# Performance work log

Hardware: AMD Instinct MI355X
Metric: run time of the kernel (lower is better)

The kernel has to match this reference:

```python
import jax, jax.numpy as jnp
import numpy as np

K = 20          # num neighbors (init kwarg k)
BN_EPS = 1e-5   # PyTorch BatchNorm default eps


def setup_inputs() -> dict:
    key = jax.random.key(0)
    k1, k2 = jax.random.split(key, 2)
    x = jax.random.normal(k1, (8, 64, 4096), dtype=jnp.float32)       # (b, d, n)
    w = jax.random.normal(k2, (64, 128), dtype=jnp.float32) * 0.05    # Conv2d 1x1: (out=64, in=2*64)
    gamma = jnp.ones((64,), jnp.float32)    # BatchNorm1d weight
    beta = jnp.zeros((64,), jnp.float32)    # BatchNorm1d bias
    return {"x": x, "w": w, "gamma": gamma, "beta": beta}


def reference(x, w, gamma, beta):
    # x: (b, d, n)
    xt = jnp.swapaxes(x, 1, 2)                       # (b, n, d)
    # kNN via pairwise squared euclidean distance (same ordering as torch.cdist)
    sq = jnp.sum(xt * xt, axis=-1)                   # (b, n)
    d2 = sq[:, :, None] + sq[:, None, :] - 2.0 * jnp.einsum('bnd,bmd->bnm', xt, xt)
    _, idx = jax.lax.top_k(-d2, K)                   # (b, n, K) smallest distances
    # gather neighbor features: (b, n, K, d)
    nb = jax.vmap(lambda pts, i: pts[i])(xt, idx)
    ctr = xt[:, :, None, :]                          # (b, n, 1, d)
    # edge feature = concat([neighbor - x, x]) -> (b, n, K, 2d)
    feat = jnp.concatenate([nb - ctr, jnp.broadcast_to(ctr, nb.shape)], axis=-1)
    # 1x1 conv (no bias) then max over neighbors
    h = jnp.max(jnp.einsum('bnkc,oc->bnko', feat, w), axis=2)   # (b, n, out)
    # BatchNorm1d (training mode: batch statistics over (b, n), biased var)
    mean = jnp.mean(h, axis=(0, 1))
    var = jnp.mean((h - mean) ** 2, axis=(0, 1))
    hn = (h - mean) / jnp.sqrt(var + BN_EPS) * gamma + beta
    out = jax.nn.gelu(hn, approximate=False)         # exact GELU (PyTorch default)
    return jnp.swapaxes(out, 1, 2)                   # (b, out, n)
```

## Files before the change

### kernel.cpp

```cpp
#include <hip/hip_runtime.h>

#define BIGF 3.402823466e38f

typedef __attribute__((ext_vector_type(8))) short bf16x8;
typedef __attribute__((ext_vector_type(4))) float f32x4;

__device__ __forceinline__ void gload_lds16u(const unsigned short* g, unsigned short* lds) {
  __builtin_amdgcn_global_load_lds((const __attribute__((address_space(1))) void*)g,
                                   (__attribute__((address_space(3))) void*)lds, 16, 0, 0);
}

__device__ __forceinline__ unsigned short bf16_rne(float f) {
  unsigned int u = __float_as_uint(f);
  return (unsigned short)((u + 0x7fffu + ((u >> 16) & 1u)) >> 16);
}

__global__ __launch_bounds__(256) void k1_pre(const float* __restrict__ x, const float* __restrict__ w,
                                              float* __restrict__ sq, float* __restrict__ y,
                                              float* __restrict__ delta, unsigned short* __restrict__ xhl) {
  __shared__ __align__(16) float xt[64][68];
  __shared__ __align__(16) float ws[128][64];
  const int t = threadIdx.x;
  const int bid = blockIdx.x;
  const int b = bid >> 6;
  const int n0 = (bid & 63) << 6;
  const float* xb = x + (size_t)b * 64 * 4096;

#pragma unroll
  for (int rep = 0; rep < 16; ++rep) {
    int id = rep * 256 + t;
    int d = id >> 6, n = id & 63;
    xt[n][d] = xb[(size_t)d * 4096 + n0 + n];
  }
#pragma unroll
  for (int rep = 0; rep < 32; ++rep) {
    int id = rep * 256 + t;
    int u = id >> 6, dd = id & 63;
    ws[u][dd] = w[(u & 63) * 128 + ((u >> 6) << 6) + dd];
  }
  __syncthreads();

  {
    const int p = t >> 2;
    const int cg = t & 3;
    uint4* orow = (uint4*)xhl + ((size_t)(b << 12) + n0 + p) * 16;
#pragma unroll
    for (int cc = 0; cc < 4; ++cc) {
      const int c = cg * 4 + cc;
      const int kb = (c & 7) * 8;
      const bool lohalf = (c >= 8);
      unsigned int pk[4];
#pragma unroll
      for (int j2 = 0; j2 < 4; ++j2) {
        unsigned short u0, u1;
#pragma unroll
        for (int e = 0; e < 2; ++e) {
          const float xv = xt[p][kb + j2 * 2 + e];
          unsigned short h = bf16_rne(xv);
          unsigned short r;
          if (!lohalf) r = h;
          else r = bf16_rne(xv - __uint_as_float(((unsigned int)h) << 16));
          if (e == 0) u0 = r; else u1 = r;
        }
        pk[j2] = (unsigned int)u0 | ((unsigned int)u1 << 16);
      }
      uint4 v;
      v.x = pk[0]; v.y = pk[1]; v.z = pk[2]; v.w = pk[3];
      orow[c ^ (p & 7)] = v;
    }
  }

  const int p = t & 63;
  const int oc = t >> 6;
  float accy[16], accz[16];
#pragma unroll
  for (int j = 0; j < 16; ++j) { accy[j] = 0.f; accz[j] = 0.f; }

#pragma unroll 4
  for (int d4 = 0; d4 < 16; ++d4) {
    const float4 xv = *(const float4*)&xt[p][d4 * 4];
#pragma unroll
    for (int j = 0; j < 16; ++j) {
      const int o = oc * 16 + j;
      const float4 wy = *(const float4*)&ws[o][d4 * 4];
      const float4 wz = *(const float4*)&ws[o + 64][d4 * 4];
      accy[j] = fmaf(xv.x, wy.x, fmaf(xv.y, wy.y, fmaf(xv.z, wy.z, fmaf(xv.w, wy.w, accy[j]))));
      accz[j] = fmaf(xv.x, wz.x, fmaf(xv.y, wz.y, fmaf(xv.z, wz.z, fmaf(xv.w, wz.w, accz[j]))));
    }
  }

  if (oc == 0) {
    float s = 0.f;
#pragma unroll
    for (int d4 = 0; d4 < 16; ++d4) {
      const float4 v = *(const float4*)&xt[p][d4 * 4];
      s = fmaf(v.x, v.x, fmaf(v.y, v.y, fmaf(v.z, v.z, fmaf(v.w, v.w, s))));
    }
    sq[b * 4096 + n0 + p] = s;
  }

  const size_t row = ((size_t)b * 4096 + n0 + p) * 64 + oc * 16;
#pragma unroll
  for (int j4 = 0; j4 < 4; ++j4) {
    float4 yv = make_float4(accy[j4 * 4], accy[j4 * 4 + 1], accy[j4 * 4 + 2], accy[j4 * 4 + 3]);
    float4 dv = make_float4(accz[j4 * 4] - accy[j4 * 4], accz[j4 * 4 + 1] - accy[j4 * 4 + 1],
                            accz[j4 * 4 + 2] - accy[j4 * 4 + 2], accz[j4 * 4 + 3] - accy[j4 * 4 + 3]);
    *(float4*)&y[row + j4 * 4] = yv;
    *(float4*)&delta[row + j4 * 4] = dv;
  }
}

__global__ __launch_bounds__(256, 2) void k2_knn(const unsigned short* __restrict__ xhl,
                                                 const float* __restrict__ sq,
                                                 int* __restrict__ idx_out) {
  __shared__ __align__(16) float smem[15424];
  const int t = threadIdx.x;
  const int lane = t & 63;
  const int w = t >> 6;
  float* BsW = smem + 4096 + (w << 11);
  uint4* BsW4 = (uint4*)BsW;
  const uint4* As4 = (const uint4*)smem;
  unsigned* bufD = (unsigned*)smem;
  unsigned* bufI = (unsigned*)(smem + 12288);
  unsigned* thrNa = (unsigned*)(smem + 15360);
  volatile unsigned* thrNv = (volatile unsigned*)(smem + 15360);

  const int bid = blockIdx.x;
  const int b = bid >> 6;
  const int n0 = (bid & 63) << 6;
  const int pn = lane & 15, q = lane >> 4;
  const int myn = lane;
  const int swz = myn & 7;

  const unsigned short* xr = xhl + ((size_t)(b << 12)) * 128;
  const float* sqb = sq + (b << 12);

  if (t < 64) thrNa[t] = 0x7F7FFFFFu;

  {
    unsigned short* asu = (unsigned short*)smem;
#pragma unroll
    for (int qq = 0; qq < 4; ++qq) {
      const int kk = w * 4 + qq;
      gload_lds16u(xr + (size_t)n0 * 128 + kk * 512 + lane * 8, asu + kk * 512);
    }
  }
  const float sqn = sqb[n0 + myn];
  __builtin_amdgcn_s_waitcnt(0x0F70);
  __syncthreads();

  bf16x8 bfr[4][4];
#pragma unroll
  for (int nt = 0; nt < 4; ++nt)
#pragma unroll
    for (int j = 0; j < 4; ++j)
      bfr[nt][j] = *reinterpret_cast<const bf16x8*>(&As4[((nt << 4) + pn) * 16 + (((j << 2) + q) ^ (pn & 7))]);
  __syncthreads();

  float kd[20];
  int ki[20];
#pragma unroll
  for (int s = 0; s < 20; ++s) { kd[s] = BIGF; ki[s] = -1; }
  int cnt = 0;

  auto ins = [&](float vd, int vi) {
#pragma unroll
    for (int s = 19; s >= 1; --s) {
      const bool a = vd < kd[s - 1];
      const bool bb = vd < kd[s];
      kd[s] = a ? kd[s - 1] : (bb ? vd : kd[s]);
      ki[s] = a ? ki[s - 1] : (bb ? vi : ki[s]);
    }
    const bool b0 = vd < kd[0];
    kd[0] = b0 ? vd : kd[0];
    ki[0] = b0 ? vi : ki[0];
  };

  auto drain = [&]() {
    unsigned vD[12], vI[12];
#pragma unroll
    for (int j = 0; j < 12; ++j) { vD[j] = bufD[j * 256 + t]; vI[j] = bufI[j * 256 + t]; }
#pragma unroll
    for (int j = 0; j < 12; ++j) {
      if (__any(j < cnt)) {
        if (j < cnt) {
          const float dv = __uint_as_float(vD[j]);
          if (dv < kd[19]) ins(dv, (int)vI[j]);
        }
      }
    }
    cnt = 0;
    atomicMin(&thrNa[myn], __float_as_uint(kd[19]));
  };

  const f32x4 zero4 = {0.f, 0.f, 0.f, 0.f};
  f32x4 acc[4][2];
#pragma unroll
  for (int nt = 0; nt < 4; ++nt) { acc[nt][0] = zero4; acc[nt][1] = zero4; }

  for (int kt = 0; kt < 32; ++kt) {
    const int mbase = (w + 4 * kt) << 5;
    {
      unsigned short* bsu = (unsigned short*)BsW;
      const unsigned short* src = xr + (size_t)mbase * 128;
#pragma unroll
      for (int k = 0; k < 8; ++k) gload_lds16u(src + k * 512 + lane * 8, bsu + k * 512);
    }
    const f32x4 sqm0 = *(const f32x4*)&sqb[mbase + (q << 2)];
    const f32x4 sqm1 = *(const f32x4*)&sqb[mbase + 16 + (q << 2)];
    __builtin_amdgcn_s_waitcnt(0x0F70);

    float thr2 = (fminf(__uint_as_float(thrNv[myn]), kd[19]) - sqn) + 0.001f;

#pragma unroll
    for (int mt = 0; mt < 2; ++mt) {
      bf16x8 afr[4];
#pragma unroll
      for (int j = 0; j < 4; ++j)
        afr[j] = *reinterpret_cast<const bf16x8*>(&BsW4[((mt << 4) + pn) * 16 + (((j << 2) + q) ^ (pn & 7))]);
#pragma unroll
      for (int nt = 0; nt < 4; ++nt) {
        f32x4 a = acc[nt][mt];
        a = __builtin_amdgcn_mfma_f32_16x16x32_bf16(afr[0], bfr[nt][0], a, 0, 0, 0);
        a = __builtin_amdgcn_mfma_f32_16x16x32_bf16(afr[1], bfr[nt][1], a, 0, 0, 0);
        a = __builtin_amdgcn_mfma_f32_16x16x32_bf16(afr[0], bfr[nt][2], a, 0, 0, 0);
        a = __builtin_amdgcn_mfma_f32_16x16x32_bf16(afr[1], bfr[nt][3], a, 0, 0, 0);
        a = __builtin_amdgcn_mfma_f32_16x16x32_bf16(afr[2], bfr[nt][0], a, 0, 0, 0);
        a = __builtin_amdgcn_mfma_f32_16x16x32_bf16(afr[3], bfr[nt][1], a, 0, 0, 0);
        acc[nt][mt] = a;
      }
    }

#pragma unroll
    for (int nt = 0; nt < 4; ++nt) {
#pragma unroll
      for (int mt = 0; mt < 2; ++mt) {
        const int n = (nt << 4) + pn;
        const int g = (mt << 2) + q;
        const int pc = g ^ (n & 7);
        const f32x4 sv = mt ? sqm1 : sqm0;
        f32x4 dv = sv - 2.0f * acc[nt][mt];
        *(f32x4*)&BsW[(n << 5) + (pc << 2)] = dv;
        acc[nt][mt] = zero4;
      }
    }

#pragma unroll 1
    for (int half = 0; half < 2; ++half) {
      const int cb = half << 2;
      const float4 v0 = *(const float4*)&BsW[(myn << 5) + (((cb + 0) ^ swz) << 2)];
      const float4 v1 = *(const float4*)&BsW[(myn << 5) + (((cb + 1) ^ swz) << 2)];
      const float4 v2 = *(const float4*)&BsW[(myn << 5) + (((cb + 2) ^ swz) << 2)];
      const float4 v3 = *(const float4*)&BsW[(myn << 5) + (((cb + 3) ^ swz) << 2)];
#pragma unroll
      for (int cc = 0; cc < 4; ++cc) {
        const float4 v = (cc == 0) ? v0 : (cc == 1) ? v1 : (cc == 2) ? v2 : v3;
        const int mb = mbase + ((cb + cc) << 2);
        const float mn = fminf(fminf(v.x, v.y), fminf(v.z, v.w));
        if (mn < thr2) {
          if (v.x < thr2) { bufD[cnt * 256 + t] = __float_as_uint(sqn + v.x); bufI[cnt * 256 + t] = (unsigned)mb; cnt++; }
          if (v.y < thr2) { bufD[cnt * 256 + t] = __float_as_uint(sqn + v.y); bufI[cnt * 256 + t] = (unsigned)(mb + 1); cnt++; }
          if (v.z < thr2) { bufD[cnt * 256 + t] = __float_as_uint(sqn + v.z); bufI[cnt * 256 + t] = (unsigned)(mb + 2); cnt++; }
          if (v.w < thr2) { bufD[cnt * 256 + t] = __float_as_uint(sqn + v.w); bufI[cnt * 256 + t] = (unsigned)(mb + 3); cnt++; }
        }
        if (__any(cnt > 8)) {
          drain();
          thr2 = fminf(thr2, (fminf(__uint_as_float(thrNv[myn]), kd[19]) - sqn) + 0.001f);
        }
      }
    }
  }
  drain();

  __syncthreads();
  float* pf = smem;
  int* pi = (int*)(smem + 5120);
#pragma unroll
  for (int s = 0; s < 20; ++s) {
    pf[(w * 20 + s) * 64 + lane] = kd[s];
    pi[(w * 20 + s) * 64 + lane] = ki[s];
  }
  __syncthreads();
  if (w == 0) {
    auto insTie = [&](float vd, int vi) {
#pragma unroll
      for (int s = 0; s < 20; ++s) {
        const float od = kd[s];
        const int oi = ki[s];
        const bool lt = (vd < od) || (vd == od && vi < oi);
        kd[s] = lt ? vd : od;
        ki[s] = lt ? vi : oi;
        vd = lt ? od : vd;
        vi = lt ? oi : vi;
      }
    };
    for (int ww = 1; ww < 4; ++ww) {
#pragma unroll 1
      for (int s = 0; s < 20; ++s) {
        const float dv = pf[(ww * 20 + s) * 64 + lane];
        const int iv = pi[(ww * 20 + s) * 64 + lane];
        if (dv < kd[19] || (dv == kd[19] && iv < ki[19])) insTie(dv, iv);
      }
    }
    int* orow = idx_out + ((size_t)(b << 12) + n0 + lane) * 20;
#pragma unroll
    for (int s = 0; s < 20; ++s) orow[s] = ki[s];
  }
}

__global__ __launch_bounds__(256) void k3_gather(const float* __restrict__ y,
                                                 const float* __restrict__ delta,
                                                 const int* __restrict__ idx,
                                                 float* __restrict__ h,
                                                 float* __restrict__ sums,
                                                 float* __restrict__ sumsq) {
  const int t = threadIdx.x;
  const int lane = t & 63;
  const int w = t >> 6;
  const int blk = blockIdx.x;
  float s1 = 0.f, s2 = 0.f;
  for (int p = 0; p < 16; ++p) {
    const int ng = blk * 64 + w * 16 + p;
    const int b = ng >> 12;
    const int* row = idx + (size_t)ng * 20;
    float mx = -BIGF;
#pragma unroll
    for (int kk = 0; kk < 20; ++kk) {
      const int nbr = row[kk];
      mx = fmaxf(mx, y[((size_t)(b << 12) + nbr) * 64 + lane]);
    }
    const float hv = mx + delta[(size_t)ng * 64 + lane];
    h[(size_t)ng * 64 + lane] = hv;
    s1 += hv;
    s2 += hv * hv;
  }
  __shared__ float r1[4][64], r2[4][64];
  r1[w][lane] = s1;
  r2[w][lane] = s2;
  __syncthreads();
  if (w == 0) {
    const float a = r1[0][lane] + r1[1][lane] + r1[2][lane] + r1[3][lane];
    const float c = r2[0][lane] + r2[1][lane] + r2[2][lane] + r2[3][lane];
    atomicAdd(&sums[lane], a);
    atomicAdd(&sumsq[lane], c);
  }
}

__global__ __launch_bounds__(256) void k4_bn(const float* __restrict__ h,
                                             const float* __restrict__ sums,
                                             const float* __restrict__ sumsq,
                                             const float* __restrict__ gamma,
                                             const float* __restrict__ beta,
                                             float* __restrict__ out) {
  __shared__ float tile[64][65];
  const int bid = blockIdx.x;
  const int b = bid >> 6;
  const int n0 = (bid & 63) << 6;
  const int t = threadIdx.x;
  const int o = t & 63;
#pragma unroll
  for (int it = 0; it < 16; ++it) {
    const int n = (t >> 6) * 16 + it;
    tile[n][o] = h[(((size_t)b << 12) + n0 + n) * 64 + o];
  }
  __syncthreads();
  const int j = t & 63;
#pragma unroll
  for (int it = 0; it < 16; ++it) {
    const int oo = (t >> 6) * 16 + it;
    const float mean = sums[oo] * (1.0f / 32768.0f);
    const float var = sumsq[oo] * (1.0f / 32768.0f) - mean * mean;
    const float sc = gamma[oo] / sqrtf(var + 1e-5f);
    const float hv = tile[j][oo];
    const float hn = (hv - mean) * sc + beta[oo];
    const float g = 0.5f * hn * (1.0f + erff(hn * 0.70710678118654752f));
    out[((size_t)(b * 64 + oo)) * 4096 + n0 + j] = g;
  }
}

extern "C" void kernel_launch(void* const* d_in, const int* in_sizes, int n_in,
                              void* d_out, int out_size, void* d_ws, size_t ws_size,
                              hipStream_t stream) {
  const float* x = (const float*)d_in[0];
  const float* w = (const float*)d_in[1];
  const float* gamma = (const float*)d_in[2];
  const float* beta = (const float*)d_in[3];
  float* out = (float*)d_out;

  float* sq_ws = (float*)d_ws;
  float* y_ws = sq_ws + 32768;
  float* delta_ws = y_ws + 2097152;
  float* h_ws = delta_ws + 2097152;
  int* idx_ws = (int*)(h_ws + 2097152);
  float* sums = (float*)(idx_ws + 655360);
  float* sumsq = sums + 64;
  unsigned short* xhl = (unsigned short*)h_ws;

  hipMemsetAsync(sums, 0, 2 * 64 * sizeof(float), stream);
  k1_pre<<<512, 256, 0, stream>>>(x, w, sq_ws, y_ws, delta_ws, xhl);
  k2_knn<<<512, 256, 0, stream>>>(xhl, sq_ws, idx_ws);
  k3_gather<<<512, 256, 0, stream>>>(y_ws, delta_ws, idx_ws, h_ws, sums, sumsq);
  k4_bn<<<512, 256, 0, stream>>>(h_ws, sums, sumsq, gamma, beta, out);
}
```

Baseline: 314.9 us.

## Prefetch next neighbor tile into LDS during distance computation in kNN kernel

```diff
diff --git a/kernel.cpp b/kernel.cpp
--- a/kernel.cpp
+++ b/kernel.cpp
@@ -113,17 +113,18 @@
 __global__ __launch_bounds__(256, 2) void k2_knn(const unsigned short* __restrict__ xhl,
                                                  const float* __restrict__ sq,
                                                  int* __restrict__ idx_out) {
-  __shared__ __align__(16) float smem[15424];
+  __shared__ __align__(16) float smem[20480];
   const int t = threadIdx.x;
   const int lane = t & 63;
   const int w = t >> 6;
   float* BsW = smem + 4096 + (w << 11);
+  float* DpW = smem + 12288 + (w << 11);
   uint4* BsW4 = (uint4*)BsW;
   const uint4* As4 = (const uint4*)smem;
   unsigned* bufD = (unsigned*)smem;
-  unsigned* bufI = (unsigned*)(smem + 12288);
-  unsigned* thrNa = (unsigned*)(smem + 15360);
-  volatile unsigned* thrNv = (volatile unsigned*)(smem + 15360);
+  unsigned* bufI = (unsigned*)(smem + 1536);
+  unsigned* thrNa = (unsigned*)(smem + 3072);
+  volatile unsigned* thrNv = (volatile unsigned*)(smem + 3072);
 
   const int bid = blockIdx.x;
   const int b = bid >> 6;
@@ -135,8 +136,6 @@
   const unsigned short* xr = xhl + ((size_t)(b << 12)) * 128;
   const float* sqb = sq + (b << 12);
 
-  if (t < 64) thrNa[t] = 0x7F7FFFFFu;
-
   {
     unsigned short* asu = (unsigned short*)smem;
 #pragma unroll
@@ -144,7 +143,13 @@
       const int kk = w * 4 + qq;
       gload_lds16u(xr + (size_t)n0 * 128 + kk * 512 + lane * 8, asu + kk * 512);
     }
-  }
+    unsigned short* bsu = (unsigned short*)BsW;
+    const unsigned short* src = xr + (size_t)(w << 5) * 128;
+#pragma unroll
+    for (int k = 0; k < 8; ++k) gload_lds16u(src + k * 512 + lane * 8, bsu + k * 512);
+  }
+  f32x4 sqm0 = *(const f32x4*)&sqb[(w << 5) + (q << 2)];
+  f32x4 sqm1 = *(const f32x4*)&sqb[(w << 5) + 16 + (q << 2)];
   const float sqn = sqb[n0 + myn];
   __builtin_amdgcn_s_waitcnt(0x0F70);
   __syncthreads();
@@ -157,11 +162,13 @@
       bfr[nt][j] = *reinterpret_cast<const bf16x8*>(&As4[((nt << 4) + pn) * 16 + (((j << 2) + q) ^ (pn & 7))]);
   __syncthreads();
 
+  if (t < 64) thrNa[t] = 0x7F7FFFFFu;
   float kd[20];
   int ki[20];
 #pragma unroll
   for (int s = 0; s < 20; ++s) { kd[s] = BIGF; ki[s] = -1; }
   int cnt = 0;
+  __syncthreads();
 
   auto ins = [&](float vd, int vi) {
 #pragma unroll
@@ -177,11 +184,11 @@
   };
 
   auto drain = [&]() {
-    unsigned vD[12], vI[12];
-#pragma unroll
-    for (int j = 0; j < 12; ++j) { vD[j] = bufD[j * 256 + t]; vI[j] = bufI[j * 256 + t]; }
-#pragma unroll
-    for (int j = 0; j < 12; ++j) {
+    unsigned vD[6], vI[6];
+#pragma unroll
+    for (int j = 0; j < 6; ++j) { vD[j] = bufD[j * 256 + t]; vI[j] = bufI[j * 256 + t]; }
+#pragma unroll
+    for (int j = 0; j < 6; ++j) {
       if (__any(j < cnt)) {
         if (j < cnt) {
           const float dv = __uint_as_float(vD[j]);
@@ -197,38 +204,51 @@
   f32x4 acc[4][2];
 #pragma unroll
   for (int nt = 0; nt < 4; ++nt) { acc[nt][0] = zero4; acc[nt][1] = zero4; }
+  f32x4 sqmN0 = zero4, sqmN1 = zero4;
 
   for (int kt = 0; kt < 32; ++kt) {
     const int mbase = (w + 4 * kt) << 5;
-    {
+    __builtin_amdgcn_s_waitcnt(0x0F70);
+
+    float thr2 = (fminf(__uint_as_float(thrNv[myn]), kd[19]) - sqn) + 0.001f;
+
+    bf16x8 afr0[4], afr1[4];
+#pragma unroll
+    for (int j = 0; j < 4; ++j)
+      afr0[j] = *reinterpret_cast<const bf16x8*>(&BsW4[(pn)*16 + (((j << 2) + q) ^ (pn & 7))]);
+#pragma unroll
+    for (int j = 0; j < 4; ++j)
+      afr1[j] = *reinterpret_cast<const bf16x8*>(&BsW4[(16 + pn) * 16 + (((j << 2) + q) ^ (pn & 7))]);
+    __builtin_amdgcn_s_waitcnt(0xC07F);
+
+    if (kt < 31) {
+      const int mbn = (w + 4 * (kt + 1)) << 5;
       unsigned short* bsu = (unsigned short*)BsW;
-      const unsigned short* src = xr + (size_t)mbase * 128;
+      const unsigned short* src = xr + (size_t)mbn * 128;
 #pragma unroll
       for (int k = 0; k < 8; ++k) gload_lds16u(src + k * 512 + lane * 8, bsu + k * 512);
-    }
-    const f32x4 sqm0 = *(const f32x4*)&sqb[mbase + (q << 2)];
-    const f32x4 sqm1 = *(const f32x4*)&sqb[mbase + 16 + (q << 2)];
-    __builtin_amdgcn_s_waitcnt(0x0F70);
-
-    float thr2 = (fminf(__uint_as_float(thrNv[myn]), kd[19]) - sqn) + 0.001f;
-
-#pragma unroll
-    for (int mt = 0; mt < 2; ++mt) {
-      bf16x8 afr[4];
-#pragma unroll
-      for (int j = 0; j < 4; ++j)
-        afr[j] = *reinterpret_cast<const bf16x8*>(&BsW4[((mt << 4) + pn) * 16 + (((j << 2) + q) ^ (pn & 7))]);
-#pragma unroll
-      for (int nt = 0; nt < 4; ++nt) {
-        f32x4 a = acc[nt][mt];
-        a = __builtin_amdgcn_mfma_f32_16x16x32_bf16(afr[0], bfr[nt][0], a, 0, 0, 0);
-        a = __builtin_amdgcn_mfma_f32_16x16x32_bf16(afr[1], bfr[nt][1], a, 0, 0, 0);
-        a = __builtin_amdgcn_mfma_f32_16x16x32_bf16(afr[0], bfr[nt][2], a, 0, 0, 0);
-        a = __builtin_amdgcn_mfma_f32_16x16x32_bf16(afr[1], bfr[nt][3], a, 0, 0, 0);
-        a = __builtin_amdgcn_mfma_f32_16x16x32_bf16(afr[2], bfr[nt][0], a, 0, 0, 0);
-        a = __builtin_amdgcn_mfma_f32_16x16x32_bf16(afr[3], bfr[nt][1], a, 0, 0, 0);
-        acc[nt][mt] = a;
-      }
+      sqmN0 = *(const f32x4*)&sqb[mbn + (q << 2)];
+      sqmN1 = *(const f32x4*)&sqb[mbn + 16 + (q << 2)];
+    }
+
+#pragma unroll
+    for (int nt = 0; nt < 4; ++nt) {
+      f32x4 a = acc[nt][0];
+      a = __builtin_amdgcn_mfma_f32_16x16x32_bf16(afr0[0], bfr[nt][0], a, 0, 0, 0);
+      a = __builtin_amdgcn_mfma_f32_16x16x32_bf16(afr0[1], bfr[nt][1], a, 0, 0, 0);
+      a = __builtin_amdgcn_mfma_f32_16x16x32_bf16(afr0[0], bfr[nt][2], a, 0, 0, 0);
+      a = __builtin_amdgcn_mfma_f32_16x16x32_bf16(afr0[1], bfr[nt][3], a, 0, 0, 0);
+      a = __builtin_amdgcn_mfma_f32_16x16x32_bf16(afr0[2], bfr[nt][0], a, 0, 0, 0);
+      a = __builtin_amdgcn_mfma_f32_16x16x32_bf16(afr0[3], bfr[nt][1], a, 0, 0, 0);
+      acc[nt][0] = a;
+      f32x4 c = acc[nt][1];
+      c = __builtin_amdgcn_mfma_f32_16x16x32_bf16(afr1[0], bfr[nt][0], c, 0, 0, 0);
+      c = __builtin_amdgcn_mfma_f32_16x16x32_bf16(afr1[1], bfr[nt][1], c, 0, 0, 0);
+      c = __builtin_amdgcn_mfma_f32_16x16x32_bf16(afr1[0], bfr[nt][2], c, 0, 0, 0);
+      c = __builtin_amdgcn_mfma_f32_16x16x32_bf16(afr1[1], bfr[nt][3], c, 0, 0, 0);
+      c = __builtin_amdgcn_mfma_f32_16x16x32_bf16(afr1[2], bfr[nt][0], c, 0, 0, 0);
+      c = __builtin_amdgcn_mfma_f32_16x16x32_bf16(afr1[3], bfr[nt][1], c, 0, 0, 0);
+      acc[nt][1] = c;
     }
 
 #pragma unroll
@@ -240,7 +260,7 @@
         const int pc = g ^ (n & 7);
         const f32x4 sv = mt ? sqm1 : sqm0;
         f32x4 dv = sv - 2.0f * acc[nt][mt];
-        *(f32x4*)&BsW[(n << 5) + (pc << 2)] = dv;
+        *(f32x4*)&DpW[(n << 5) + (pc << 2)] = dv;
         acc[nt][mt] = zero4;
       }
     }
@@ -248,10 +268,10 @@
 #pragma unroll 1
     for (int half = 0; half < 2; ++half) {
       const int cb = half << 2;
-      const float4 v0 = *(const float4*)&BsW[(myn << 5) + (((cb + 0) ^ swz) << 2)];
-      const float4 v1 = *(const float4*)&BsW[(myn << 5) + (((cb + 1) ^ swz) << 2)];
-      const float4 v2 = *(const float4*)&BsW[(myn << 5) + (((cb + 2) ^ swz) << 2)];
-      const float4 v3 = *(const float4*)&BsW[(myn << 5) + (((cb + 3) ^ swz) << 2)];
+      const float4 v0 = *(const float4*)&DpW[(myn << 5) + (((cb + 0) ^ swz) << 2)];
+      const float4 v1 = *(const float4*)&DpW[(myn << 5) + (((cb + 1) ^ swz) << 2)];
+      const float4 v2 = *(const float4*)&DpW[(myn << 5) + (((cb + 2) ^ swz) << 2)];
+      const float4 v3 = *(const float4*)&DpW[(myn << 5) + (((cb + 3) ^ swz) << 2)];
 #pragma unroll
       for (int cc = 0; cc < 4; ++cc) {
         const float4 v = (cc == 0) ? v0 : (cc == 1) ? v1 : (cc == 2) ? v2 : v3;
@@ -263,12 +283,14 @@
           if (v.z < thr2) { bufD[cnt * 256 + t] = __float_as_uint(sqn + v.z); bufI[cnt * 256 + t] = (unsigned)(mb + 2); cnt++; }
           if (v.w < thr2) { bufD[cnt * 256 + t] = __float_as_uint(sqn + v.w); bufI[cnt * 256 + t] = (unsigned)(mb + 3); cnt++; }
         }
-        if (__any(cnt > 8)) {
+        if (__any(cnt > 2)) {
           drain();
           thr2 = fminf(thr2, (fminf(__uint_as_float(thrNv[myn]), kd[19]) - sqn) + 0.001f);
         }
       }
     }
+    sqm0 = sqmN0;
+    sqm1 = sqmN1;
   }
   drain();
 
```

New measurement: 357.2 us. +13.4%, slower.
